# Performance work log

Measured on AMD Instinct MI355X. Metric: run time of the kernel, lower is better.

## Reference

```python
import jax, jax.numpy as jnp
import numpy as np

B, D, H, E, K = 4096, 2048, 2048, 8, 2

def setup_inputs() -> dict:
    key = jax.random.key(0)
    k1, k2, k3 = jax.random.split(key, 3)
    x = jax.random.normal(k1, (B, D), dtype=jnp.float32)
    # keras RandomNormal(stddev=0.001) init for gating and expert kernels, zero bias
    Wg = jax.random.normal(k2, (D, E), dtype=jnp.float32) * 0.001
    bg = jnp.zeros((E,), dtype=jnp.float32)
    We = jax.random.normal(k3, (E, D, H), dtype=jnp.float32) * 0.001
    be = jnp.zeros((E, H), dtype=jnp.float32)
    return {"x": x, "Wg": Wg, "bg": bg, "We": We, "be": be}

def reference(x, Wg, bg, We, be):
    # softmax gating: [B, E]
    gating = jax.nn.softmax(x @ Wg + bg, axis=-1)
    # top-k expert selection
    topk_w, topk_idx = jax.lax.top_k(gating, K)        # [B, K]
    # dense expert stack (module runs all experts): [B, E, H]
    expert_out = jnp.einsum('bd,edh->beh', x, We) + be[None, :, :]
    # gather_nd equivalent: pick top-k experts per token -> [B, K, H]
    topk_out = jnp.take_along_axis(expert_out, topk_idx[:, :, None], axis=1)
    # weighted combine: [B, H]
    combined = jnp.sum(topk_out * topk_w[:, :, None], axis=1)
    return combined
```

## Files before the change

### kernel.cpp

```cpp
#include <hip/hip_runtime.h>
#include <hip/hip_bf16.h>
#include <stdint.h>
#include <stddef.h>

#define B_TOK 4096
#define D_DIM 2048
#define H_DIM 2048
#define E_NUM 8
#define MAX_SLOTS 72

typedef __bf16 bf16;
typedef __attribute__((ext_vector_type(8))) __bf16 bf16x8;
typedef __attribute__((ext_vector_type(4))) __bf16 bf16x4;
typedef __attribute__((ext_vector_type(4))) float f32x4;

#define WS_COUNTS   0
#define WS_ENTRIES  4096
#define WS_TKIDX    135168
#define WS_TKW      167936
#define WS_XBF      262144
#define WS_WET      17039360
#define WS_AUX      84148224ULL
#define WS_BIG_NEED 84148224ULL
#define WS_SPLIT_NEED 117702656ULL

__device__ __forceinline__ void gload16(const void* g, void* l) {
  __builtin_amdgcn_global_load_lds(
      (const __attribute__((address_space(1))) void*)g,
      (__attribute__((address_space(3))) void*)l, 16, 0, 0);
}

__global__ void zero_counts(int* counts) {
  counts[threadIdx.x] = 0;
}


__global__ __launch_bounds__(256) void gating_dot(
    const float* __restrict__ x,
    const float* __restrict__ Wg,
    const float* __restrict__ bg,
    int* __restrict__ tk_idx, float* __restrict__ tk_w) {
  int gtid = blockIdx.x * blockDim.x + threadIdx.x;
  int b = gtid >> 6;
  int lane = threadIdx.x & 63;
  if (b >= B_TOK) return;
  const float* xrow = x + (size_t)b * D_DIM;

  float acc[E_NUM];
#pragma unroll
  for (int e = 0; e < E_NUM; e++) acc[e] = 0.f;

#pragma unroll
  for (int i = 0; i < 8; i++) {
    int d0 = i * 256 + lane * 4;
    f32x4 xv = *(const f32x4*)(xrow + d0);
#pragma unroll
    for (int j = 0; j < 4; j++) {
      float xf = xv[j];
      f32x4 w0 = *(const f32x4*)(Wg + (size_t)(d0 + j) * E_NUM);
      f32x4 w1 = *(const f32x4*)(Wg + (size_t)(d0 + j) * E_NUM + 4);
#pragma unroll
      for (int e = 0; e < 4; e++) acc[e] += xf * w0[e];
#pragma unroll
      for (int e = 0; e < 4; e++) acc[4 + e] += xf * w1[e];
    }
  }
#pragma unroll
  for (int e = 0; e < E_NUM; e++) {
    float v = acc[e];
#pragma unroll
    for (int off = 32; off >= 1; off >>= 1) v += __shfl_xor(v, off, 64);
    acc[e] = v;
  }

  if (lane == 0) {
    float lg[E_NUM];
#pragma unroll
    for (int e = 0; e < E_NUM; e++) lg[e] = acc[e] + bg[e];
    int i0 = 0; float v0 = lg[0];
#pragma unroll
    for (int e = 1; e < E_NUM; e++) if (lg[e] > v0) { v0 = lg[e]; i0 = e; }
    int i1 = -1; float v1 = -1e30f;
#pragma unroll
    for (int e = 0; e < E_NUM; e++)
      if (e != i0 && lg[e] > v1) { v1 = lg[e]; i1 = e; }
    float m = v0;
    float den = 0.f, p0 = 0.f, p1 = 0.f;
#pragma unroll
    for (int e = 0; e < E_NUM; e++) {
      float pe = expf(lg[e] - m);
      den += pe;
      if (e == i0) p0 = pe;
      if (e == i1) p1 = pe;
    }
    tk_idx[2 * b] = i0;
    tk_idx[2 * b + 1] = i1;
    tk_w[2 * b] = p0 / den;
    tk_w[2 * b + 1] = p1 / den;
  }
}

__global__ __launch_bounds__(256) void xcvt_kernel(const float* __restrict__ x,
                                                   bf16* __restrict__ xbf) {
  int idx = blockIdx.x * blockDim.x + threadIdx.x;
  f32x4 a = *(const f32x4*)(x + (size_t)idx * 8);
  f32x4 c = *(const f32x4*)(x + (size_t)idx * 8 + 4);
  bf16x8 o;
#pragma unroll
  for (int j = 0; j < 4; j++) { o[j] = (bf16)a[j]; o[4 + j] = (bf16)c[j]; }
  *(bf16x8*)(xbf + (size_t)idx * 8) = o;
}

__global__ __launch_bounds__(256) void prefill_kernel(
    const float* __restrict__ be,
    const int* __restrict__ tk_idx,
    const float* __restrict__ tk_w,
    float* __restrict__ out) {
  int idx = blockIdx.x * blockDim.x + threadIdx.x;
  int b = idx >> 9;
  int hc = (idx & 511) * 4;
  int e0 = tk_idx[2 * b], e1 = tk_idx[2 * b + 1];
  float w0 = tk_w[2 * b], w1 = tk_w[2 * b + 1];
  f32x4 b0 = *(const f32x4*)(be + (size_t)e0 * H_DIM + hc);
  f32x4 b1 = *(const f32x4*)(be + (size_t)e1 * H_DIM + hc);
  f32x4 o;
#pragma unroll
  for (int j = 0; j < 4; j++) o[j] = w0 * b0[j] + w1 * b1[j];
  *(f32x4*)(out + (size_t)b * H_DIM + hc) = o;
}

__global__ __launch_bounds__(256) void bucketize_kernel(
    const int* __restrict__ tk_idx, int* counts, int* entries) {
  __shared__ int cursor_s;
  __shared__ int base_s;
  int e = blockIdx.x >> 3, chunk = blockIdx.x & 7;
  int tid = threadIdx.x;
  if (tid == 0) cursor_s = 0;
  __syncthreads();

  int flat[4]; bool m[4]; int nm = 0;
#pragma unroll
  for (int j = 0; j < 4; j++) {
    flat[j] = chunk * 1024 + j * 256 + tid;
    int ee = tk_idx[flat[j]];
    m[j] = (ee == e);
    nm += m[j] ? 1 : 0;
  }
  int my_off = atomicAdd(&cursor_s, nm);
  __syncthreads();
  if (tid == 0) base_s = atomicAdd(&counts[e * 16], cursor_s);
  __syncthreads();
  int p = base_s + my_off;
#pragma unroll
  for (int j = 0; j < 4; j++)
    if (m[j]) entries[e * B_TOK + p++] = flat[j];
}

__global__ void transpose_cvt_we(const float* __restrict__ We, bf16* __restrict__ WeT) {
  __shared__ __align__(16) float tile[64][65];
  int e = blockIdx.z;
  int h0 = blockIdx.x * 64, d0 = blockIdx.y * 64;
  int t = threadIdx.x;
  int dr = t >> 2, hc = (t & 3) * 16;
  const float* src = We + ((size_t)e * D_DIM + d0 + dr) * H_DIM + h0 + hc;
#pragma unroll
  for (int i = 0; i < 4; i++)
    *(f32x4*)(&tile[dr][hc + 4 * i]) = *(const f32x4*)(src + 4 * i);
  __syncthreads();
  int lane = t & 63, w = t >> 6;
#pragma unroll
  for (int s = 0; s < 2; s++) {
    int c = w * 2 + s;
    int n16 = c & 3, kslab = c >> 2;
    int nl = n16 * 16 + (lane & 15);
    int kl = kslab * 32 + (lane >> 4) * 8;
    bf16x8 v;
#pragma unroll
    for (int j = 0; j < 8; j++) v[j] = (bf16)tile[kl + j][nl];
    int gh = h0 + nl, gd = d0 + kl;
    int ntile = gh >> 7, n = gh & 127;
    int k0 = gd >> 5;
    size_t slab = ((size_t)((e * 16 + ntile) * 64 + k0)) * 4096;
    int off = ((n >> 4) * 512) + lane * 8;
    *(bf16x8*)(WeT + slab + off) = v;
  }
}

__global__ __launch_bounds__(256) void moe_gemm_fast(
    const bf16* __restrict__ xbf, const bf16* __restrict__ WeT,
    const int* __restrict__ counts, const int* __restrict__ entries,
    const float* __restrict__ tk_w, float* __restrict__ out,
    float* __restrict__ aux) {
  __shared__ __align__(16) bf16 As_s[3 * 4096];
  __shared__ __align__(16) bf16 Bs_s[3 * 4096];
  int bid = blockIdx.x;
  int slot = bid >> 4, ntile = bid & 15;
  int e = -1, toff = 0, cnt = 0;
  {
    int tot = 0;
#pragma unroll
    for (int i = 0; i < E_NUM; i++) {
      int c = counts[i * 16];
      int t = (c + 127) >> 7;
      if (slot >= tot && slot < tot + t) { e = i; toff = tot; cnt = c; }
      tot += t;
    }
  }
  if (e < 0) return;
  int mtile = slot - toff;
  int n0 = ntile * 128;
  int tid = threadIdx.x, lane = tid & 63, w = tid >> 6;
  int r = lane & 15, q = lane >> 4;
  const int* ereg = entries + e * B_TOK;
  const bf16* wet_nt = WeT + ((size_t)(e * 16 + ntile) * 64) * 4096;

  const bf16* srcA[2];
  const bf16* srcB[2];
  int chunk_off[2];
#pragma unroll
  for (int j = 0; j < 2; j++) {
    int ci = w * 2 + j;
    int m = mtile * 128 + 16 * ci + r;
    int tok = ereg[min(m, cnt - 1)] >> 1;
    srcA[j] = xbf + (size_t)tok * D_DIM + 8 * q;
    chunk_off[j] = ci * 512;
    srcB[j] = wet_nt + chunk_off[j] + lane * 8;
  }
  int wm4 = (w & 1) * 4, wn4 = (w >> 1) * 4;

  f32x4 acc[4][4];
#pragma unroll
  for (int i = 0; i < 4; i++)
#pragma unroll
    for (int j = 0; j < 4; j++) acc[i][j] = (f32x4){0.f, 0.f, 0.f, 0.f};

#pragma unroll
  for (int p = 0; p < 2; p++) {
#pragma unroll
    for (int j = 0; j < 2; j++) {
      gload16(srcA[j] + p * 32, As_s + p * 4096 + chunk_off[j]);
      gload16(srcB[j] + p * 4096, Bs_s + p * 4096 + chunk_off[j]);
    }
  }

  int pc = 0, pb = 2;
  for (int it = 0; it < 63; it++) {
    asm volatile("s_waitcnt vmcnt(4)\n\ts_barrier" ::: "memory");
    if (it < 62) {
      int kk = (it + 2) * 32;
#pragma unroll
      for (int j = 0; j < 2; j++) {
        gload16(srcA[j] + kk, As_s + pb * 4096 + chunk_off[j]);
        gload16(srcB[j] + (size_t)(it + 2) * 4096, Bs_s + pb * 4096 + chunk_off[j]);
      }
    }
    {
      const bf16* Ab = As_s + pc * 4096;
      const bf16* Bb = Bs_s + pc * 4096;
      bf16x8 af[4], bfr[4];
#pragma unroll
      for (int i = 0; i < 4; i++)
        af[i] = *(const bf16x8*)(Ab + (wm4 + i) * 512 + lane * 8);
#pragma unroll
      for (int j = 0; j < 4; j++)
        bfr[j] = *(const bf16x8*)(Bb + (wn4 + j) * 512 + lane * 8);
#pragma unroll
      for (int i = 0; i < 4; i++)
#pragma unroll
        for (int j = 0; j < 4; j++)
          acc[i][j] = __builtin_amdgcn_mfma_f32_16x16x32_bf16(af[i], bfr[j],
                                                              acc[i][j], 0, 0, 0);
    }
    pc = (pc == 2) ? 0 : pc + 1;
    pb = (pb == 2) ? 0 : pb + 1;
  }
  asm volatile("s_waitcnt vmcnt(0)\n\ts_barrier" ::: "memory");
  {
    const bf16* Ab = As_s + pc * 4096;
    const bf16* Bb = Bs_s + pc * 4096;
    bf16x8 af[4], bfr[4];
#pragma unroll
    for (int i = 0; i < 4; i++)
      af[i] = *(const bf16x8*)(Ab + (wm4 + i) * 512 + lane * 8);
#pragma unroll
    for (int j = 0; j < 4; j++)
      bfr[j] = *(const bf16x8*)(Bb + (wn4 + j) * 512 + lane * 8);
#pragma unroll
    for (int i = 0; i < 4; i++)
#pragma unroll
      for (int j = 0; j < 4; j++)
        acc[i][j] = __builtin_amdgcn_mfma_f32_16x16x32_bf16(af[i], bfr[j],
                                                            acc[i][j], 0, 0, 0);
  }

  int base_r = mtile * 128, wm = (w & 1) * 64, wn = (w >> 1) * 64;
#pragma unroll
  for (int i = 0; i < 4; i++)
#pragma unroll
    for (int reg = 0; reg < 4; reg++) {
      int rg = base_r + wm + 16 * i + q * 4 + reg;
      if (rg < cnt) {
        int ent = ereg[rg];
        int tok = ent >> 1, slotk = ent & 1;
        float wgt = tk_w[2 * tok + slotk];
        if (aux) {
          float* dst = (slotk ? aux : out) + (size_t)tok * H_DIM + n0 + wn;
#pragma unroll
          for (int j = 0; j < 4; j++)
            dst[16 * j + r] = wgt * acc[i][j][reg];
        } else {
          float* orow = out + (size_t)tok * H_DIM + n0 + wn;
#pragma unroll
          for (int j = 0; j < 4; j++)
            atomicAdd(orow + 16 * j + r, wgt * acc[i][j][reg]);
        }
      }
    }
}

__global__ __launch_bounds__(256) void combine_kernel(
    const float* __restrict__ aux,
    const float* __restrict__ be,
    const int* __restrict__ tk_idx,
    const float* __restrict__ tk_w,
    float* __restrict__ out) {
  int w = threadIdx.x >> 6, lane = threadIdx.x & 63;
  int b = blockIdx.x * 4 + w;
  int e0 = tk_idx[2 * b], e1 = tk_idx[2 * b + 1];
  float w0 = tk_w[2 * b], w1 = tk_w[2 * b + 1];
  const float* be0 = be + (size_t)e0 * H_DIM;
  const float* be1 = be + (size_t)e1 * H_DIM;
  const float* arow = aux + (size_t)b * H_DIM;
  float* orow = out + (size_t)b * H_DIM;
#pragma unroll
  for (int c = 0; c < 8; c++) {
    int h = c * 256 + lane * 4;
    f32x4 o = *(const f32x4*)(orow + h);
    f32x4 a = *(const f32x4*)(arow + h);
    f32x4 v0 = *(const f32x4*)(be0 + h);
    f32x4 v1 = *(const f32x4*)(be1 + h);
#pragma unroll
    for (int j = 0; j < 4; j++) o[j] = o[j] + a[j] + w0 * v0[j] + w1 * v1[j];
    *(f32x4*)(orow + h) = o;
  }
}

__global__ __launch_bounds__(256) void moe_gemm_slow(
    const float* __restrict__ x, const float* __restrict__ We,
    const int* __restrict__ counts, const int* __restrict__ entries,
    const float* __restrict__ tk_w, float* __restrict__ out) {
  __shared__ __align__(16) bf16 As_f[4096];
  __shared__ __align__(16) bf16 Bs_f[4096];
  __shared__ __align__(16) float Braw[4096];
  int e = blockIdx.y >> 5, mtile = blockIdx.y & 31;
  int cnt = counts[e * 16];
  if (mtile * 128 >= cnt) return;
  int n0 = blockIdx.x * 128;
  int tid = threadIdx.x, lane = tid & 63, w = tid >> 6;
  int r = lane & 15, q = lane >> 4;
  const int* ereg = entries + e * B_TOK;

  const float* srcA[2]; bf16* dstA[2];
#pragma unroll
  for (int s = 0; s < 2; s++) {
    int c = tid + s * 256;
    int ci = c >> 6, qq = (c >> 4) & 3, rr = c & 15;
    int m = mtile * 128 + 16 * ci + rr;
    int tok = ereg[min(m, cnt - 1)] >> 1;
    srcA[s] = x + (size_t)tok * D_DIM + 8 * qq;
    dstA[s] = As_f + c * 8;
  }
  const float* srcBr[4]; float* dstBr[4];
#pragma unroll
  for (int i = 0; i < 4; i++) {
    int row = (w * 4 + i) * 2 + (lane >> 5);
    srcBr[i] = We + ((size_t)e * D_DIM + row) * H_DIM + n0 + (lane & 31) * 4;
    dstBr[i] = Braw + (w * 4 + i) * 256;
  }
  int n2[2], q2[2]; bf16* dstB2[2];
#pragma unroll
  for (int s = 0; s < 2; s++) {
    int c = tid + s * 256;
    n2[s] = 16 * (c >> 6) + (c & 15);
    q2[s] = (c >> 4) & 3;
    dstB2[s] = Bs_f + c * 8;
  }
  int wm4 = (w & 1) * 4, wn4 = (w >> 1) * 4;

  f32x4 acc[4][4];
#pragma unroll
  for (int i = 0; i < 4; i++)
#pragma unroll
    for (int j = 0; j < 4; j++) acc[i][j] = (f32x4){0.f, 0.f, 0.f, 0.f};

  for (int k0 = 0; k0 < D_DIM; k0 += 32) {
    __syncthreads();
#pragma unroll
    for (int i = 0; i < 4; i++)
      gload16(srcBr[i] + (size_t)k0 * H_DIM, dstBr[i]);
#pragma unroll
    for (int s = 0; s < 2; s++) {
      f32x4 a0 = *(const f32x4*)(srcA[s] + k0);
      f32x4 a1 = *(const f32x4*)(srcA[s] + k0 + 4);
      bf16x8 av;
#pragma unroll
      for (int j = 0; j < 4; j++) { av[j] = (bf16)a0[j]; av[4 + j] = (bf16)a1[j]; }
      *(bf16x8*)dstA[s] = av;
    }
    __syncthreads();
#pragma unroll
    for (int s = 0; s < 2; s++) {
      bf16x8 bv;
#pragma unroll
      for (int t2 = 0; t2 < 8; t2++)
        bv[t2] = (bf16)Braw[(8 * q2[s] + t2) * 128 + n2[s]];
      *(bf16x8*)dstB2[s] = bv;
    }
    __syncthreads();
    bf16x8 af[4], bfr[4];
#pragma unroll
    for (int i = 0; i < 4; i++)
      af[i] = *(const bf16x8*)(As_f + (wm4 + i) * 512 + lane * 8);
#pragma unroll
    for (int j = 0; j < 4; j++)
      bfr[j] = *(const bf16x8*)(Bs_f + (wn4 + j) * 512 + lane * 8);
#pragma unroll
    for (int i = 0; i < 4; i++)
#pragma unroll
      for (int j = 0; j < 4; j++)
        acc[i][j] = __builtin_amdgcn_mfma_f32_16x16x32_bf16(af[i], bfr[j],
                                                            acc[i][j], 0, 0, 0);
  }

  int base_r = mtile * 128, wm = (w & 1) * 64, wn = (w >> 1) * 64;
#pragma unroll
  for (int i = 0; i < 4; i++)
#pragma unroll
    for (int reg = 0; reg < 4; reg++) {
      int rg = base_r + wm + 16 * i + q * 4 + reg;
      if (rg < cnt) {
        int ent = ereg[rg];
        int tok = ent >> 1, slotk = ent & 1;
        float wgt = tk_w[2 * tok + slotk];
        float* orow = out + (size_t)tok * H_DIM + n0 + wn;
#pragma unroll
        for (int j = 0; j < 4; j++)
          atomicAdd(orow + 16 * j + r, wgt * acc[i][j][reg]);
      }
    }
}

extern "C" void kernel_launch(void* const* d_in, const int* in_sizes, int n_in,
                              void* d_out, int out_size, void* d_ws, size_t ws_size,
                              hipStream_t stream) {
  const float* x  = (const float*)d_in[0];
  const float* Wg = (const float*)d_in[1];
  const float* bg = (const float*)d_in[2];
  const float* We = (const float*)d_in[3];
  const float* be = (const float*)d_in[4];
  float* out = (float*)d_out;

  char* ws = (char*)d_ws;
  int*   counts   = (int*)(ws + WS_COUNTS);
  int*   entries  = (int*)(ws + WS_ENTRIES);
  int*   tk_idx   = (int*)(ws + WS_TKIDX);
  float* tk_w     = (float*)(ws + WS_TKW);
  bf16*  xbf      = (bf16*)(ws + WS_XBF);
  bf16*  WeT      = (bf16*)(ws + WS_WET);
  float* aux      = (float*)(ws + WS_AUX);

  bool big   = (ws_size >= WS_BIG_NEED);
  bool split = (ws_size >= WS_SPLIT_NEED);

  hipLaunchKernelGGL(zero_counts, dim3(1), dim3(128), 0, stream, counts);
  hipLaunchKernelGGL(gating_dot, dim3(B_TOK / 4), dim3(256), 0, stream,
                     x, Wg, bg, tk_idx, tk_w);
  hipLaunchKernelGGL(bucketize_kernel, dim3(64), dim3(256), 0, stream,
                     tk_idx, counts, entries);
  if (big) {
    hipLaunchKernelGGL(xcvt_kernel, dim3(B_TOK * D_DIM / 8 / 256), dim3(256), 0,
                       stream, x, xbf);
    if (!split)
      hipLaunchKernelGGL(prefill_kernel, dim3(B_TOK * H_DIM / 4 / 256), dim3(256),
                         0, stream, be, tk_idx, tk_w, out);
    hipLaunchKernelGGL(transpose_cvt_we, dim3(H_DIM / 64, D_DIM / 64, E_NUM),
                       dim3(256), 0, stream, We, WeT);
    hipLaunchKernelGGL(moe_gemm_fast, dim3(MAX_SLOTS * 16), dim3(256), 0, stream,
                       xbf, WeT, counts, entries, tk_w, out,
                       split ? aux : (float*)nullptr);
    if (split)
      hipLaunchKernelGGL(combine_kernel, dim3(B_TOK / 4), dim3(256), 0, stream,
                         aux, be, tk_idx, tk_w, out);
  } else {
    hipLaunchKernelGGL(prefill_kernel, dim3(B_TOK * H_DIM / 4 / 256), dim3(256),
                       0, stream, be, tk_idx, tk_w, out);
    hipLaunchKernelGGL(moe_gemm_slow, dim3(H_DIM / 128, E_NUM * 32), dim3(256), 0,
                       stream, x, We, counts, entries, tk_w, out);
  }
}
```

Before: 434.8 us.

## Fuse x bf16 conversion into gating kernel and process 8 tokens per block

The gating kernel now handles 8 tokens per block, and each thread keeps its slice of Wg in registers so the gate weights are reused across those tokens. The same pass converts x to bf16 and writes xbf, so the separate xcvt_kernel launch and its second read of x are removed. Partial sums are reduced with shuffles plus shared memory. The cost is much higher register pressure (64 accumulators plus 64 weight floats per thread) and fewer blocks in flight.

```diff
diff --git a/kernel.cpp b/kernel.cpp
--- a/kernel.cpp
+++ b/kernel.cpp
@@ -34,49 +34,89 @@
   counts[threadIdx.x] = 0;
 }
 
-
 __global__ __launch_bounds__(256) void gating_dot(
     const float* __restrict__ x,
     const float* __restrict__ Wg,
     const float* __restrict__ bg,
-    int* __restrict__ tk_idx, float* __restrict__ tk_w) {
-  int gtid = blockIdx.x * blockDim.x + threadIdx.x;
-  int b = gtid >> 6;
-  int lane = threadIdx.x & 63;
-  if (b >= B_TOK) return;
-  const float* xrow = x + (size_t)b * D_DIM;
-
-  float acc[E_NUM];
-#pragma unroll
-  for (int e = 0; e < E_NUM; e++) acc[e] = 0.f;
-
-#pragma unroll
-  for (int i = 0; i < 8; i++) {
-    int d0 = i * 256 + lane * 4;
-    f32x4 xv = *(const f32x4*)(xrow + d0);
+    int* __restrict__ tk_idx, float* __restrict__ tk_w,
+    bf16* __restrict__ xbf) {
+  __shared__ __align__(16) float part[64][68];
+  __shared__ float tot[64];
+  int tid = threadIdx.x;
+  int b0 = blockIdx.x * 8;
+
+  f32x4 wg[16];
+  {
+    const float* wgp = Wg + (size_t)tid * 64;
+#pragma unroll
+    for (int i = 0; i < 16; i++) wg[i] = *(const f32x4*)(wgp + 4 * i);
+  }
+
+  float acc[8][8];
+#pragma unroll
+  for (int tk = 0; tk < 8; tk++)
+#pragma unroll
+    for (int e = 0; e < 8; e++) acc[tk][e] = 0.f;
+
+#pragma unroll
+  for (int tk = 0; tk < 8; tk++) {
+    const float* xr = x + (size_t)(b0 + tk) * D_DIM + tid * 8;
+    f32x4 xa = *(const f32x4*)xr;
+    f32x4 xc = *(const f32x4*)(xr + 4);
+    if (xbf) {
+      bf16x4 ba, bb;
+#pragma unroll
+      for (int j = 0; j < 4; j++) { ba[j] = (bf16)xa[j]; bb[j] = (bf16)xc[j]; }
+      bf16* xo = xbf + (size_t)(b0 + tk) * D_DIM + tid * 8;
+      *(bf16x4*)xo = ba;
+      *(bf16x4*)(xo + 4) = bb;
+    }
 #pragma unroll
     for (int j = 0; j < 4; j++) {
-      float xf = xv[j];
-      f32x4 w0 = *(const f32x4*)(Wg + (size_t)(d0 + j) * E_NUM);
-      f32x4 w1 = *(const f32x4*)(Wg + (size_t)(d0 + j) * E_NUM + 4);
-#pragma unroll
-      for (int e = 0; e < 4; e++) acc[e] += xf * w0[e];
-#pragma unroll
-      for (int e = 0; e < 4; e++) acc[4 + e] += xf * w1[e];
-    }
-  }
-#pragma unroll
-  for (int e = 0; e < E_NUM; e++) {
-    float v = acc[e];
-#pragma unroll
-    for (int off = 32; off >= 1; off >>= 1) v += __shfl_xor(v, off, 64);
-    acc[e] = v;
-  }
-
-  if (lane == 0) {
+#pragma unroll
+      for (int e = 0; e < 4; e++) {
+        acc[tk][e]     += xa[j] * wg[2 * j][e];
+        acc[tk][e + 4] += xa[j] * wg[2 * j + 1][e];
+        acc[tk][e]     += xc[j] * wg[2 * j + 8][e];
+        acc[tk][e + 4] += xc[j] * wg[2 * j + 9][e];
+      }
+    }
+  }
+
+  int lane = tid & 63, w = tid >> 6;
+#pragma unroll
+  for (int tk = 0; tk < 8; tk++)
+#pragma unroll
+    for (int e = 0; e < 8; e++) {
+      float v = acc[tk][e];
+      v += __shfl_xor(v, 1, 64);
+      v += __shfl_xor(v, 2, 64);
+      if ((lane & 3) == 0)
+        part[tk * 8 + e][w * 16 + (lane >> 2)] = v;
+    }
+  __syncthreads();
+
+  {
+    int p = tid >> 2, q = tid & 3;
+    f32x4 s4 = (f32x4){0.f, 0.f, 0.f, 0.f};
+#pragma unroll
+    for (int i = 0; i < 4; i++) {
+      f32x4 v = *(const f32x4*)&part[p][q * 16 + 4 * i];
+#pragma unroll
+      for (int j = 0; j < 4; j++) s4[j] += v[j];
+    }
+    float s = (s4[0] + s4[1]) + (s4[2] + s4[3]);
+    s += __shfl_xor(s, 1, 64);
+    s += __shfl_xor(s, 2, 64);
+    if (q == 0) tot[p] = s;
+  }
+  __syncthreads();
+
+  if (tid < 8) {
+    int b = b0 + tid;
     float lg[E_NUM];
 #pragma unroll
-    for (int e = 0; e < E_NUM; e++) lg[e] = acc[e] + bg[e];
+    for (int e = 0; e < E_NUM; e++) lg[e] = tot[tid * 8 + e] + bg[e];
     int i0 = 0; float v0 = lg[0];
 #pragma unroll
     for (int e = 1; e < E_NUM; e++) if (lg[e] > v0) { v0 = lg[e]; i0 = e; }
@@ -98,17 +138,6 @@
     tk_w[2 * b] = p0 / den;
     tk_w[2 * b + 1] = p1 / den;
   }
-}
-
-__global__ __launch_bounds__(256) void xcvt_kernel(const float* __restrict__ x,
-                                                   bf16* __restrict__ xbf) {
-  int idx = blockIdx.x * blockDim.x + threadIdx.x;
-  f32x4 a = *(const f32x4*)(x + (size_t)idx * 8);
-  f32x4 c = *(const f32x4*)(x + (size_t)idx * 8 + 4);
-  bf16x8 o;
-#pragma unroll
-  for (int j = 0; j < 4; j++) { o[j] = (bf16)a[j]; o[4 + j] = (bf16)c[j]; }
-  *(bf16x8*)(xbf + (size_t)idx * 8) = o;
 }
 
 __global__ __launch_bounds__(256) void prefill_kernel(
@@ -473,13 +502,11 @@
   bool split = (ws_size >= WS_SPLIT_NEED);
 
   hipLaunchKernelGGL(zero_counts, dim3(1), dim3(128), 0, stream, counts);
-  hipLaunchKernelGGL(gating_dot, dim3(B_TOK / 4), dim3(256), 0, stream,
-                     x, Wg, bg, tk_idx, tk_w);
+  hipLaunchKernelGGL(gating_dot, dim3(B_TOK / 8), dim3(256), 0, stream,
+                     x, Wg, bg, tk_idx, tk_w, big ? xbf : (bf16*)nullptr);
   hipLaunchKernelGGL(bucketize_kernel, dim3(64), dim3(256), 0, stream,
                      tk_idx, counts, entries);
   if (big) {
-    hipLaunchKernelGGL(xcvt_kernel, dim3(B_TOK * D_DIM / 8 / 256), dim3(256), 0,
-                       stream, x, xbf);
     if (!split)
       hipLaunchKernelGGL(prefill_kernel, dim3(B_TOK * H_DIM / 4 / 256), dim3(256),
                          0, stream, be, tk_idx, tk_w, out);
```

Result: faster. 410.7 us (-5.5%).
